# Optimization experiments

Measured on AMD Instinct MI355X. Metric: run time of the kernel, lower is better.

The kernel has to match this reference:

```python
import jax, jax.numpy as jnp
import numpy as np
from jax import lax

B, T, N, D = 4, 12, 1024, 128
C_FRONT = 78           # front/back channel split used by the mixup
X_LAST = T // 2 - 1    # static row index of the last (only effective) mixup call
BS_ST = 6              # block_size of mixup_region_ST
SIGMA = 10.0
LN_EPS = 1e-5


def _mixup_region_ST(graph, y):
    """Faithful jax port of mixup_region_ST(graph_front, x=X_LAST, y, 6, sigma=10).
    graph: [T, N, C_FRONT] float; y: traced int scalar."""
    T_, N_, C_ = graph.shape
    x = X_LAST  # static python int
    y_start = jnp.maximum(y - BS_ST, 0)
    y_end = jnp.minimum(y + 2 * BS_ST, N_)

    # temporal gaussian mix of column y over rows [0, x), written at (x, y)
    xs = jnp.arange(x, dtype=graph.dtype)
    w = jnp.exp(-((xs - (x - 1.0)) ** 2) / (2.0 * SIGMA ** 2))
    w = w / w.sum()
    target = graph[:x, y, :]                      # [x, C]
    mixed_value = (w[:, None] * target).sum(0)    # [C]
    g = lax.dynamic_update_slice(graph, mixed_value[None, None, :], (x, y, 0))

    def mix_write(g_, bs, maxj):
        # average blocks g_[:, j*bs:(j+1)*bs, :] for j in [y_start//bs, y_end//bs)
        j0 = y_start // bs
        j1 = y_end // bs
        jj = jnp.arange(maxj)
        mask = (jj < (j1 - j0)).astype(g_.dtype)              # [maxj]
        cols = jnp.clip((j0 + jj)[:, None] * bs + jnp.arange(bs)[None, :], 0, N_ - 1)
        blocks = g_[:, cols, :]                               # [T, maxj, bs, C]
        mixed = (blocks * mask[None, :, None, None]).sum(1) / (j1 - j0).astype(g_.dtype)
        # torch writes mixed_region.to(torch.uint8) into a float tensor
        mixed = lax.stop_gradient(mixed.astype(jnp.uint8).astype(g_.dtype))
        return lax.dynamic_update_slice(g_, mixed, (0, y, 0))

    # torch resets block_size to 1 when y_end > w - block_size
    return lax.cond(y_end > N_ - BS_ST,
                    lambda g_: mix_write(g_, 1, 3 * BS_ST),
                    lambda g_: mix_write(g_, BS_ST, 4),
                    g)


def _forward(inp, adapt_G, xff_w, xff_b, ff1_w, ff1_b, ff2_w, ff2_b, ln_w, ln_b):
    x_ = inp @ xff_w.T + xff_b                       # [B,T,N,3D]
    q, k, v = jnp.split(x_, 3, axis=-1)
    e = jnp.einsum('btnd,btmd->btnm', q, k) / (D ** 0.5)
    e = e @ adapt_G                                  # [B,T,N,N]
    attn = jax.nn.softmax(e, axis=-1)
    attn_det = lax.stop_gradient(attn)               # self.attention_maps = attn.detach()

    def process(attn_b, val_b):                      # [T,N,N], [T,N,D]
        front = val_b[..., :C_FRONT]
        back = val_b[..., C_FRONT:]
        col_sums = attn_b.sum(axis=1)                # [T, N]
        _, idx = lax.top_k(-col_sums, 2)             # 2 smallest per row, ascending
        # only the last loop iteration's mixup survives in the original code
        y = idx[X_LAST, 1]
        return jnp.concatenate([_mixup_region_ST(front, y), back], axis=-1)

    new_value = jax.vmap(process)(attn_det, v)       # [B,T,N,D]
    vi = attn @ new_value                            # [B,T,N,D]
    h = jax.nn.gelu(vi @ ff1_w.T + ff1_b, approximate=False)
    h = h @ ff2_w.T + ff2_b
    out = h + inp
    mu = out.mean(-1, keepdims=True)
    var = ((out - mu) ** 2).mean(-1, keepdims=True)
    return (out - mu) / jnp.sqrt(var + LN_EPS) * ln_w + ln_b


def setup_inputs() -> dict:
    key = jax.random.key(0)
    ks = jax.random.split(key, 6)
    s = 0.02
    return {
        'input': jax.random.normal(ks[0], (B, T, N, D), jnp.float32),
        'adapt_G': jax.random.normal(ks[1], (N, N), jnp.float32) / np.float32(np.sqrt(N)),
        'xff_w': jax.random.normal(ks[2], (3 * D, D), jnp.float32) * s,
        'xff_b': jnp.zeros((3 * D,), jnp.float32),
        'ff1_w': jax.random.normal(ks[3], (D, D), jnp.float32) * s,
        'ff1_b': jnp.zeros((D,), jnp.float32),
        'ff2_w': jax.random.normal(ks[4], (D, D), jnp.float32) * s,
        'ff2_b': jnp.zeros((D,), jnp.float32),
        'ln_w': jnp.ones((D,), jnp.float32),
        'ln_b': jnp.zeros((D,), jnp.float32),
    }


def reference(input, adapt_G, xff_w, xff_b, ff1_w, ff1_b, ff2_w, ff2_b, ln_w, ln_b):
    return _forward(input, adapt_G, xff_w, xff_b, ff1_w, ff1_b, ff2_w, ff2_b, ln_w, ln_b)
```

## Files before the change

### kernel.cpp

```cpp
#include <hip/hip_runtime.h>
#include <hip/hip_bf16.h>

typedef __attribute__((ext_vector_type(8))) short bf16x8;
typedef __attribute__((ext_vector_type(4))) float f32x4;
typedef unsigned long long ull;

#define MFMA(a,b,c) __builtin_amdgcn_mfma_f32_16x16x32_bf16((a),(b),(c),0,0,0)
#define VMCNT(N) asm volatile("s_waitcnt vmcnt(%0)" :: "i"(N) : "memory")

__device__ __forceinline__ short f2bs(float f){
  union { float f; unsigned u; } x; x.f = f;
  unsigned r = (x.u + 0x7fffu + ((x.u >> 16) & 1u)) >> 16;
  return (short)r;
}
__device__ __forceinline__ float bs2f(short s){
  union { unsigned u; float f; } x; x.u = ((unsigned)(unsigned short)s) << 16;
  return x.f;
}

__device__ __forceinline__ void gl2lds16(const void* g, void* l){
  __builtin_amdgcn_global_load_lds((const __attribute__((address_space(1))) void*)g,
                                   (__attribute__((address_space(3))) void*)l, 16, 0, 0);
}

__device__ __forceinline__ void merge2(ull& a1, ull& a2, ull b1, ull b2){
  ull n1 = min(a1, b1);
  ull n2 = min(max(a1, b1), min(a2, b2));
  a1 = n1; a2 = n2;
}

__global__ __launch_bounds__(256) void prep_kernel(const float* __restrict__ xffw,
                                                   const float* __restrict__ w1,
                                                   const float* __restrict__ w2,
                                                   const float* __restrict__ G,
                                                   short* __restrict__ wqkv_b,
                                                   short* __restrict__ w1_b,
                                                   short* __restrict__ w2_b,
                                                   short* __restrict__ gt){
  __shared__ float tile[32][33];
  int blk = blockIdx.x;
  if (blk >= 1024){
    int i = (blk-1024)*256 + threadIdx.x;
    int stride = 32*256;
    for (int idx = i; idx < 384*128; idx += stride) wqkv_b[idx] = f2bs(xffw[idx]);
    for (int idx = i; idx < 128*128; idx += stride) w1_b[idx] = f2bs(w1[idx]);
    for (int idx = i; idx < 128*128; idx += stride) w2_b[idx] = f2bs(w2[idx]);
    return;
  }
  int bx = blk & 31;
  int by = blk >> 5;
  int tx = threadIdx.x & 31, ty = threadIdx.x >> 5;
  #pragma unroll
  for (int j=0;j<4;j++){
    int n = by*32 + ty + j*8;
    tile[ty+j*8][tx] = G[(size_t)n*1024 + bx*32 + tx];
  }
  __syncthreads();
  #pragma unroll
  for (int j=0;j<4;j++){
    int m = bx*32 + ty + j*8;
    gt[(size_t)m*1024 + by*32 + tx] = f2bs(tile[tx][ty+j*8]);
  }
}

__global__ __launch_bounds__(256,3) void qkv_kernel(const float* __restrict__ inp,
                                                  const short* __restrict__ wqkv,
                                                  const float* __restrict__ bias,
                                                  short* __restrict__ q, short* __restrict__ kT,
                                                  short* __restrict__ nvt){
  __shared__ __align__(16) char smem[49152];
  int w = threadIdx.x >> 6, lane = threadIdx.x & 63;
  int lr = lane & 15, lg = lane >> 4;
  int r0 = blockIdx.x*64;
  int bt = blockIdx.x >> 4;
  int n0 = r0 & 1023;
  int rw = r0 + w*16;
  bf16x8 a[4];
  #pragma unroll
  for (int kc=0;kc<4;kc++){
    const float* ar = inp + (size_t)(rw+lr)*128 + kc*32 + lg*8;
    float4 f0 = *(const float4*)ar;
    float4 f1 = *(const float4*)(ar+4);
    bf16x8 t;
    t[0]=f2bs(f0.x); t[1]=f2bs(f0.y); t[2]=f2bs(f0.z); t[3]=f2bs(f0.w);
    t[4]=f2bs(f1.x); t[5]=f2bs(f1.y); t[6]=f2bs(f1.z); t[7]=f2bs(f1.w);
    a[kc]=t;
  }
  auto stageW = [&](int buf, int kc){
    #pragma unroll
    for (int t=0;t<6;t++){
      int r = (w*6+t)*16 + (lane>>2);
      int s = (lane&3) ^ ((r>>1)&3);
      gl2lds16(wqkv + (size_t)r*128 + kc*32 + s*8,
               smem + buf*24576 + (w*6+t)*1024);
    }
  };
  f32x4 acc[24];
  #pragma unroll
  for (int j=0;j<24;j++) acc[j] = f32x4{0.f,0.f,0.f,0.f};
  stageW(0, 0);
  int cur = 0;
  for (int kc=0; kc<4; kc++){
    if (kc < 3) { stageW(cur^1, kc+1); VMCNT(6); } else { VMCNT(0); }
    __builtin_amdgcn_s_barrier();
    __builtin_amdgcn_sched_barrier(0);
    const char* wb = smem + cur*24576;
    __builtin_amdgcn_s_setprio(1);
    #pragma unroll
    for (int jt=0;jt<24;jt++){
      int j = jt*16 + lr;
      bf16x8 b = *(const bf16x8*)(wb + (size_t)j*64 + ((lg ^ ((lr>>1)&3))*16));
      acc[jt] = MFMA(a[kc], b, acc[jt]);
    }
    __builtin_amdgcn_s_setprio(0);
    __builtin_amdgcn_s_barrier();
    cur ^= 1;
  }
  #pragma unroll
  for (int jt=0;jt<8;jt++){
    float bj = bias[jt*16+lr];
    #pragma unroll
    for (int rr=0;rr<4;rr++)
      q[(size_t)(rw + lg*4 + rr)*128 + jt*16 + lr] = f2bs(acc[jt][rr] + bj);
  }
  __syncthreads();
  short (*tb)[72] = (short(*)[72])smem;
  #pragma unroll
  for (int jt=8;jt<16;jt++){
    int d = (jt-8)*16 + lr;
    float bj = bias[jt*16+lr];
    #pragma unroll
    for (int rr=0;rr<4;rr++) tb[d][w*16 + lg*4 + rr] = f2bs(acc[jt][rr] + bj);
  }
  __syncthreads();
  #pragma unroll
  for (int it=0;it<4;it++){
    int idx = it*256 + threadIdx.x;
    int row = idx >> 3, c8 = (idx & 7)*8;
    *(bf16x8*)(kT + ((size_t)bt*128 + row)*1024 + n0 + c8) = *(const bf16x8*)&tb[row][c8];
  }
  __syncthreads();
  #pragma unroll
  for (int jt=16;jt<24;jt++){
    int c = (jt-16)*16 + lr;
    float bj = bias[jt*16+lr];
    #pragma unroll
    for (int rr=0;rr<4;rr++) tb[c][w*16 + lg*4 + rr] = f2bs(acc[jt][rr] + bj);
  }
  __syncthreads();
  #pragma unroll
  for (int it=0;it<4;it++){
    int idx = it*256 + threadIdx.x;
    int row = idx >> 3, c8 = (idx & 7)*8;
    *(bf16x8*)(nvt + ((size_t)bt*128 + row)*1024 + n0 + c8) = *(const bf16x8*)&tb[row][c8];
  }
}

__global__ __launch_bounds__(256,3) void kg_kernel(const short* __restrict__ gt,
                                                   const short* __restrict__ kT,
                                                   short* __restrict__ kgt){
  __shared__ __align__(16) short gtl[2][64*64];
  __shared__ __align__(16) short ktl[2][128*64];
  int lb = (blockIdx.x & 7)*96 + (blockIdx.x >> 3);
  int bt = lb >> 4;
  int mt = lb & 15;
  int w = threadIdx.x>>6, lane = threadIdx.x&63, lr = lane&15, lg = lane>>4;
  int mblk = mt*64;
  const short* kbase = kT + (size_t)bt*128*1024;
  auto stage = [&](int b, int nc){
    int n0 = nc*64;
    #pragma unroll
    for (int t=0;t<2;t++){
      int row = w*16 + t*8 + (lane>>3);
      int cswz = ((lane&7)*16) ^ ((row&7)<<4);
      gl2lds16(gt + (size_t)(mblk+row)*1024 + n0 + (cswz>>1),
               (char*)gtl[b] + w*2048 + t*1024);
    }
    #pragma unroll
    for (int t=0;t<4;t++){
      int row = w*32 + t*8 + (lane>>3);
      int cswz = ((lane&7)*16) ^ ((row&7)<<4);
      gl2lds16(kbase + (size_t)row*1024 + n0 + (cswz>>1),
               (char*)ktl[b] + w*4096 + t*1024);
    }
  };
  f32x4 acc[8];
  #pragma unroll
  for (int i=0;i<8;i++) acc[i] = f32x4{0.f,0.f,0.f,0.f};
  stage(0, 0);
  int cur = 0;
  for (int nc=0; nc<16; nc++){
    if (nc < 15) { stage(cur^1, nc+1); VMCNT(6); } else { VMCNT(0); }
    __builtin_amdgcn_s_barrier();
    __builtin_amdgcn_sched_barrier(0);
    __builtin_amdgcn_s_setprio(1);
    #pragma unroll
    for (int ks=0;ks<2;ks++){
      int arl = w*16 + lr;
      int acb = ks*64 + lg*16;
      bf16x8 af = *(const bf16x8*)((const char*)gtl[cur] + arl*128 + (acb ^ ((arl&7)<<4)));
      #pragma unroll
      for (int dt=0;dt<8;dt++){
        int brl = dt*16 + lr;
        bf16x8 bf = *(const bf16x8*)((const char*)ktl[cur] + brl*128 + (acb ^ ((brl&7)<<4)));
        acc[dt] = MFMA(af, bf, acc[dt]);
      }
    }
    __builtin_amdgcn_s_setprio(0);
    __builtin_amdgcn_s_barrier();
    cur ^= 1;
  }
  const float SCALE = 0.08838834764831845f;
  int m = mblk + w*16 + lg*4;
  #pragma unroll
  for (int dt=0;dt<8;dt++){
    #pragma unroll
    for (int rr=0;rr<4;rr++){
      kgt[((size_t)(bt*1024 + m + rr))*128 + dt*16 + lr] = f2bs(acc[dt][rr]*SCALE);
    }
  }
}

__global__ __launch_bounds__(256,4) void fused_kernel(const short* __restrict__ q,
                                                      const short* __restrict__ kgt,
                                                      const short* __restrict__ nvt,
                                                      float* __restrict__ zbuf,
                                                      short* __restrict__ pbuf,
                                                      short* __restrict__ vib){
  __shared__ __align__(16) short kgl[64*128];
  __shared__ __align__(16) short nvl[128*64];
  __shared__ __align__(16) short p_lds[4][16][64];
  int lb = (blockIdx.x & 7)*96 + (blockIdx.x >> 3);
  int bt = lb >> 4;
  int rblk = lb & 15;
  int w = threadIdx.x>>6, lane = threadIdx.x&63, lr = lane&15, lg = lane>>4;
  int r0 = rblk*64 + w*16;
  bool is5 = (bt % 12) == 5;
  int bq = bt / 12;
  const short* qrow = q + ((size_t)(bt*1024 + r0 + lr))*128;
  bf16x8 a[4];
  #pragma unroll
  for (int kc=0;kc<4;kc++) a[kc] = *(const bf16x8*)(qrow + kc*32 + lg*8);
  const short* kgb = kgt + (size_t)bt*1024*128;
  const short* nvb = nvt + (size_t)bt*128*1024;
  auto stage_kg = [&](int mc){
    int m0 = mc*64;
    #pragma unroll
    for (int t=0;t<4;t++){
      int row = w*16 + t*4 + (lane>>4);
      int cswz = ((lane&15)*16) ^ ((row&7)<<4);
      gl2lds16(kgb + (size_t)(m0+row)*128 + (cswz>>1),
               (char*)kgl + w*4096 + t*1024);
    }
  };
  auto stage_nv = [&](int mc){
    int m0 = mc*64;
    #pragma unroll
    for (int t=0;t<4;t++){
      int row = w*32 + t*8 + (lane>>3);
      int cswz = ((lane&7)*16) ^ ((row&7)<<4);
      gl2lds16(nvb + (size_t)row*1024 + m0 + (cswz>>1),
               (char*)nvl + w*4096 + t*1024);
    }
  };
  f32x4 acc[8];
  #pragma unroll
  for (int i=0;i<8;i++) acc[i] = f32x4{0.f,0.f,0.f,0.f};
  float zacc[4] = {0.f,0.f,0.f,0.f};
  stage_kg(0);
  stage_nv(0);
  VMCNT(0);
  __builtin_amdgcn_s_barrier();
  __builtin_amdgcn_sched_barrier(0);
  for (int mc=0; mc<16; mc++){
    int m0 = mc*64;
    __builtin_amdgcn_s_setprio(1);
    #pragma unroll
    for (int s=0;s<4;s++){
      f32x4 e = f32x4{0.f,0.f,0.f,0.f};
      #pragma unroll
      for (int kc=0;kc<4;kc++){
        int rl = s*16 + lr;
        int cb = kc*64 + lg*16;
        bf16x8 kb = *(const bf16x8*)((const char*)kgl + rl*256 + (cb ^ ((rl&7)<<4)));
        e = MFMA(a[kc], kb, e);
      }
      #pragma unroll
      for (int rr=0;rr<4;rr++){
        float p = __expf(fminf(e[rr], 60.f));
        zacc[rr] += p;
        p_lds[w][lg*4+rr][s*16+lr] = f2bs(p);
      }
    }
    __builtin_amdgcn_s_setprio(0);
    __builtin_amdgcn_s_barrier();
    if (mc < 15) stage_kg(mc+1);
    if (mc < 15) { VMCNT(4); } else { VMCNT(0); }
    __builtin_amdgcn_s_barrier();
    __builtin_amdgcn_sched_barrier(0);
    bf16x8 pa0 = *(const bf16x8*)&p_lds[w][lr][lg*8];
    bf16x8 pa1 = *(const bf16x8*)&p_lds[w][lr][32+lg*8];
    __builtin_amdgcn_s_setprio(1);
    #pragma unroll
    for (int ct=0; ct<8; ct++){
      int c = ct*16 + lr;
      int mb0 = lg*16;
      int mb1 = 64 + lg*16;
      bf16x8 nb0 = *(const bf16x8*)((const char*)nvl + c*128 + (mb0 ^ ((c&7)<<4)));
      bf16x8 nb1 = *(const bf16x8*)((const char*)nvl + c*128 + (mb1 ^ ((c&7)<<4)));
      acc[ct] = MFMA(pa0, nb0, acc[ct]);
      acc[ct] = MFMA(pa1, nb1, acc[ct]);
    }
    __builtin_amdgcn_s_setprio(0);
    if (is5){
      #pragma unroll
      for (int tt=0; tt<4; tt++){
        int row = tt*4 + (lane>>4);
        int m = (lane&15)*4;
        ull v = *(const ull*)&p_lds[w][row][m];
        *(ull*)(pbuf + ((size_t)bq*1024 + r0 + row)*1024 + m0 + m) = v;
      }
    }
    __builtin_amdgcn_s_barrier();
    if (mc < 15) { stage_nv(mc+1); VMCNT(4); } else { VMCNT(0); }
    __builtin_amdgcn_s_barrier();
    __builtin_amdgcn_sched_barrier(0);
  }
  #pragma unroll
  for (int d=1;d<16;d<<=1){
    #pragma unroll
    for (int rr=0;rr<4;rr++) zacc[rr] += __shfl_xor(zacc[rr], d, 64);
  }
  if (lr==0){
    #pragma unroll
    for (int rr=0;rr<4;rr++) zbuf[(size_t)bt*1024 + r0 + lg*4 + rr] = zacc[rr];
  }
  float inv[4];
  #pragma unroll
  for (int rr=0;rr<4;rr++) inv[rr] = 1.0f/zacc[rr];
  #pragma unroll
  for (int ct=0;ct<8;ct++){
    #pragma unroll
    for (int rr=0;rr<4;rr++){
      vib[((size_t)(bt*1024 + r0 + lg*4 + rr))*128 + ct*16 + lr] = f2bs(acc[ct][rr]*inv[rr]);
    }
  }
}

__global__ __launch_bounds__(256) void colsum_kernel(const short* __restrict__ pbuf,
                                                     const float* __restrict__ zbuf,
                                                     float* __restrict__ csfinal){
  __shared__ float part[4][64];
  int b = blockIdx.x >> 4, mg = blockIdx.x & 15;
  int t = threadIdx.x;
  int mcol = mg*64 + (t & 63);
  int rq = t >> 6;
  const short* pb = pbuf + (size_t)b*1024*1024;
  const float* zb = zbuf + (size_t)(b*12 + 5)*1024;
  float s = 0.f;
  for (int r = rq*256; r < rq*256 + 256; r++){
    s += bs2f(pb[(size_t)r*1024 + mcol]) * (1.0f/zb[r]);
  }
  part[rq][t & 63] = s;
  __syncthreads();
  if (t < 64){
    float cs = (part[0][t] + part[1][t]) + (part[2][t] + part[3][t]);
    csfinal[(size_t)b*1024 + mg*64 + t] = cs;
  }
}

__global__ __launch_bounds__(256) void top2_kernel(const float* __restrict__ csfinal,
                                                   int* __restrict__ yidx){
  __shared__ ull s1[4], s2[4];
  int b = blockIdx.x;
  ull b1 = ~0ull, b2 = ~0ull;
  #pragma unroll
  for (int j=0;j<4;j++){
    int col = j*256 + threadIdx.x;
    float s = csfinal[(size_t)b*1024 + col];
    union { float f; unsigned u; } cv; cv.f = s;
    ull key = ((ull)cv.u << 32) | (unsigned)col;
    merge2(b1, b2, key, ~0ull);
  }
  #pragma unroll
  for (int d=1;d<64;d<<=1){
    ull o1 = __shfl_xor(b1, d, 64);
    ull o2 = __shfl_xor(b2, d, 64);
    merge2(b1, b2, o1, o2);
  }
  int w = threadIdx.x >> 6;
  if ((threadIdx.x & 63) == 0){ s1[w] = b1; s2[w] = b2; }
  __syncthreads();
  if (threadIdx.x == 0){
    ull r1 = s1[0], r2 = s2[0];
    merge2(r1, r2, s1[1], s2[1]);
    merge2(r1, r2, s1[2], s2[2]);
    merge2(r1, r2, s1[3], s2[3]);
    yidx[b] = (int)(r2 & 0xffffffffu);
  }
}

__global__ void nvfixA_kernel(const short* __restrict__ nvt, const int* __restrict__ yidx,
                              float* __restrict__ mixres){
  int bt = blockIdx.x; int b = bt/12, t = bt%12;
  int y = yidx[b];
  int y_start = max(y-6, 0), y_end = min(y+12, 1024);
  int bs, j0, cnt;
  if (y_end > 1024-6){ bs = 1; j0 = y_start; cnt = y_end - y_start; }
  else { bs = 6; j0 = y_start/6; cnt = y_end/6 - j0; }
  int items = bs*78;
  int idx = threadIdx.x;
  if (idx >= items) return;
  int i = idx / 78, c = idx % 78;
  const short* nvb = nvt + (size_t)bt*128*1024;
  float acc = 0.f;
  for (int jj=0;jj<cnt;jj++){
    int col = (j0+jj)*bs + i;
    float gv;
    if (t == 5 && col == y){
      float wsum = 0.f, mv = 0.f;
      #pragma unroll
      for (int tp=0;tp<5;tp++){
        float d = (float)tp - 4.0f;
        float w = __expf(-d*d/200.0f);
        wsum += w;
        mv += w * bs2f(nvt[((size_t)(b*12+tp)*128 + c)*1024 + y]);
      }
      gv = mv / wsum;
    } else {
      gv = bs2f(nvb[(size_t)c*1024 + col]);
    }
    acc += gv;
  }
  mixres[((size_t)bt*6 + i)*78 + c] = acc / (float)cnt;
}

__global__ __launch_bounds__(256) void corr_kernel(const short* __restrict__ q,
                                                   const short* __restrict__ kgt,
                                                   const short* __restrict__ nvt,
                                                   const float* __restrict__ mixres,
                                                   const float* __restrict__ zbuf,
                                                   const int* __restrict__ yidx,
                                                   short* __restrict__ vib){
  __shared__ __align__(16) short kcol[6][128];
  __shared__ float delta[6][78];
  int bt = blockIdx.x >> 2;
  int rc = blockIdx.x & 3;
  int b = bt/12;
  int y = yidx[b];
  int y_end = min(y+12, 1024);
  int bs = (y_end > 1024-6) ? 1 : 6;
  for (int idx = threadIdx.x; idx < 6*128; idx += 256){
    int i = idx >> 7, d = idx & 127;
    kcol[i][d] = (i < bs) ? kgt[((size_t)(bt*1024 + y + i))*128 + d] : (short)0;
  }
  for (int idx = threadIdx.x; idx < 6*78; idx += 256){
    int i = idx / 78, c = idx % 78;
    float dv = 0.f;
    if (i < bs){
      float avg = mixres[((size_t)bt*6 + i)*78 + c];
      int ti = (int)avg;
      unsigned char u = (unsigned char)ti;
      dv = (float)u - bs2f(nvt[((size_t)bt*128 + c)*1024 + (y+i)]);
    }
    delta[i][c] = dv;
  }
  __syncthreads();
  int r = rc*256 + threadIdx.x;
  const short* qr = q + ((size_t)(bt*1024 + r))*128;
  float e[6] = {0.f,0.f,0.f,0.f,0.f,0.f};
  for (int d0 = 0; d0 < 128; d0 += 8){
    bf16x8 qv = *(const bf16x8*)(qr + d0);
    #pragma unroll
    for (int j=0;j<8;j++){
      float qf = bs2f(qv[j]);
      #pragma unroll
      for (int i=0;i<6;i++) e[i] += qf * bs2f(kcol[i][d0+j]);
    }
  }
  float invz = 1.0f / zbuf[(size_t)bt*1024 + r];
  float p[6];
  #pragma unroll
  for (int i=0;i<6;i++) p[i] = (i < bs) ? __expf(fminf(e[i],60.f))*invz : 0.f;
  short* vr = vib + ((size_t)(bt*1024 + r))*128;
  for (int c=0;c<78;c++){
    float dsum = 0.f;
    #pragma unroll
    for (int i=0;i<6;i++) dsum += p[i]*delta[i][c];
    vr[c] = f2bs(bs2f(vr[c]) + dsum);
  }
}

__global__ __launch_bounds__(256,3) void ffn_kernel(const short* __restrict__ vib,
                                                  const float* __restrict__ inp,
                                                  const short* __restrict__ w1b,
                                                  const short* __restrict__ w2b,
                                                  const float* __restrict__ b1,
                                                  const float* __restrict__ b2,
                                                  const float* __restrict__ lnw,
                                                  const float* __restrict__ lnb,
                                                  float* __restrict__ out){
  __shared__ __align__(16) short wl[128*128];
  __shared__ __align__(16) short h_lds[4][16][136];
  int w = threadIdx.x>>6, lane = threadIdx.x&63, lr = lane&15, lg = lane>>4;
  int r0 = blockIdx.x*64 + w*16;
  auto stageW = [&](const short* src){
    #pragma unroll
    for (int t=0;t<8;t++){
      int r = (w*8+t)*4 + (lane>>4);
      int s = (lane&15) ^ (r&7);
      gl2lds16(src + (size_t)r*128 + s*8, (char*)wl + (w*8+t)*1024);
    }
  };
  stageW(w1b);
  bf16x8 a[4];
  #pragma unroll
  for (int kc=0;kc<4;kc++) a[kc] = *(const bf16x8*)(vib + (size_t)(r0+lr)*128 + kc*32 + lg*8);
  __syncthreads();
  f32x4 acc[8];
  #pragma unroll
  for (int i=0;i<8;i++) acc[i] = f32x4{0.f,0.f,0.f,0.f};
  __builtin_amdgcn_s_setprio(1);
  #pragma unroll
  for (int kc=0;kc<4;kc++){
    #pragma unroll
    for (int jt=0;jt<8;jt++){
      bf16x8 b = *(const bf16x8*)((const char*)wl + (size_t)(jt*16+lr)*256 + (((kc*4+lg) ^ (lr&7))*16));
      acc[jt] = MFMA(a[kc], b, acc[jt]);
    }
  }
  __builtin_amdgcn_s_setprio(0);
  #pragma unroll
  for (int jt=0;jt<8;jt++){
    float bj = b1[jt*16+lr];
    #pragma unroll
    for (int rr=0;rr<4;rr++){
      float x = acc[jt][rr] + bj;
      float g = 0.5f*x*(1.0f + erff(x*0.70710678118654752f));
      h_lds[w][lg*4+rr][jt*16+lr] = f2bs(g);
    }
  }
  __syncthreads();
  stageW(w2b);
  bf16x8 ha[4];
  #pragma unroll
  for (int kc=0;kc<4;kc++) ha[kc] = *(const bf16x8*)&h_lds[w][lr][kc*32 + lg*8];
  __syncthreads();
  f32x4 acc2[8];
  #pragma unroll
  for (int i=0;i<8;i++) acc2[i] = f32x4{0.f,0.f,0.f,0.f};
  __builtin_amdgcn_s_setprio(1);
  #pragma unroll
  for (int kc=0;kc<4;kc++){
    #pragma unroll
    for (int jt=0;jt<8;jt++){
      bf16x8 b = *(const bf16x8*)((const char*)wl + (size_t)(jt*16+lr)*256 + (((kc*4+lg) ^ (lr&7))*16));
      acc2[jt] = MFMA(ha[kc], b, acc2[jt]);
    }
  }
  __builtin_amdgcn_s_setprio(0);
  float xv[8][4];
  #pragma unroll
  for (int jt=0;jt<8;jt++){
    float bj = b2[jt*16+lr];
    #pragma unroll
    for (int rr=0;rr<4;rr++){
      xv[jt][rr] = acc2[jt][rr] + bj + inp[(size_t)(r0 + lg*4 + rr)*128 + jt*16 + lr];
    }
  }
  float mu[4], rstd[4];
  #pragma unroll
  for (int rr=0;rr<4;rr++){
    float s = 0.f;
    #pragma unroll
    for (int jt=0;jt<8;jt++) s += xv[jt][rr];
    #pragma unroll
    for (int m=1;m<16;m<<=1) s += __shfl_xor(s, m, 64);
    mu[rr] = s * (1.0f/128.0f);
  }
  #pragma unroll
  for (int rr=0;rr<4;rr++){
    float s = 0.f;
    #pragma unroll
    for (int jt=0;jt<8;jt++){ float d = xv[jt][rr]-mu[rr]; s += d*d; }
    #pragma unroll
    for (int m=1;m<16;m<<=1) s += __shfl_xor(s, m, 64);
    rstd[rr] = rsqrtf(s * (1.0f/128.0f) + 1e-5f);
  }
  #pragma unroll
  for (int jt=0;jt<8;jt++){
    int col = jt*16 + lr;
    float lw = lnw[col], lb = lnb[col];
    #pragma unroll
    for (int rr=0;rr<4;rr++){
      out[(size_t)(r0 + lg*4 + rr)*128 + col] = (xv[jt][rr]-mu[rr])*rstd[rr]*lw + lb;
    }
  }
}

extern "C" void kernel_launch(void* const* d_in, const int* in_sizes, int n_in,
                              void* d_out, int out_size, void* d_ws, size_t ws_size,
                              hipStream_t stream) {
  (void)in_sizes; (void)n_in; (void)out_size;
  const float* inp  = (const float*)d_in[0];
  const float* G    = (const float*)d_in[1];
  const float* xffw = (const float*)d_in[2];
  const float* xffb = (const float*)d_in[3];
  const float* w1   = (const float*)d_in[4];
  const float* b1   = (const float*)d_in[5];
  const float* w2   = (const float*)d_in[6];
  const float* b2   = (const float*)d_in[7];
  const float* lnw  = (const float*)d_in[8];
  const float* lnb  = (const float*)d_in[9];
  float* out = (float*)d_out;
  char* ws = (char*)d_ws;

  size_t off = 0;
  auto take = [&](size_t bytes)->char*{ char* p = ws + off; off += (bytes + 255) & ~(size_t)255; return p; };
  short* wqkv_b = (short*)take(384*128*2);
  short* gt_b   = (short*)take((size_t)1024*1024*2);
  short* w1_b   = (short*)take(128*128*2);
  short* w2_b   = (short*)take(128*128*2);
  short* qb     = (short*)take((size_t)48*1024*128*2);
  short* kTb    = (short*)take((size_t)48*128*1024*2);
  short* nvt    = (short*)take((size_t)48*128*1024*2);
  short* kgt    = (short*)take((size_t)48*1024*128*2);
  float* zbuf   = (float*)take((size_t)48*1024*4);
  short* pbuf   = (short*)take((size_t)4*1024*1024*2);
  float* csfin  = (float*)take((size_t)4*1024*4);
  int*   yidx   = (int*)take(256);
  float* mixres = (float*)take((size_t)48*6*78*4);
  short* vibuf  = (short*)take((size_t)48*1024*128*2);
  if (off > ws_size) return;

  prep_kernel<<<dim3(1056), dim3(256), 0, stream>>>(xffw, w1, w2, G, wqkv_b, w1_b, w2_b, gt_b);
  qkv_kernel<<<dim3(768), dim3(256), 0, stream>>>(inp, wqkv_b, xffb, qb, kTb, nvt);
  kg_kernel<<<dim3(768), dim3(256), 0, stream>>>(gt_b, kTb, kgt);
  fused_kernel<<<dim3(768), dim3(256), 0, stream>>>(qb, kgt, nvt, zbuf, pbuf, vibuf);
  colsum_kernel<<<dim3(64), dim3(256), 0, stream>>>(pbuf, zbuf, csfin);
  top2_kernel<<<dim3(4), dim3(256), 0, stream>>>(csfin, yidx);
  nvfixA_kernel<<<dim3(48), dim3(512), 0, stream>>>(nvt, yidx, mixres);
  corr_kernel<<<dim3(192), dim3(256), 0, stream>>>(qb, kgt, nvt, mixres, zbuf, yidx, vibuf);
  ffn_kernel<<<dim3(768), dim3(256), 0, stream>>>(vibuf, inp, w1_b, w2_b, b1, b2, lnw, lnb, out);
}
```

Baseline: 153.5 us.

## Halve waves per block in fused attention kernel, each wave handling two row groups

The fused attention kernel now runs 128 threads (2 waves) per block instead of 4. Each wave computes 32 rows as two 16-row MFMA groups, so every K/V fragment read from LDS is reused twice. This cuts LDS reads per MFMA and barrier participants per block, and each wave issues twice as many staging loads. The P scratch buffer is now XOR-swizzled to avoid bank conflicts. In exchange, register pressure roughly doubles (two accumulator sets) and occupancy per CU drops, with launch bounds lowered to 2.

```diff
diff --git a/kernel.cpp b/kernel.cpp
--- a/kernel.cpp
+++ b/kernel.cpp
@@ -221,7 +221,7 @@
   }
 }
 
-__global__ __launch_bounds__(256,4) void fused_kernel(const short* __restrict__ q,
+__global__ __launch_bounds__(128,2) void fused_kernel(const short* __restrict__ q,
                                                       const short* __restrict__ kgt,
                                                       const short* __restrict__ nvt,
                                                       float* __restrict__ zbuf,
@@ -229,44 +229,51 @@
                                                       short* __restrict__ vib){
   __shared__ __align__(16) short kgl[64*128];
   __shared__ __align__(16) short nvl[128*64];
-  __shared__ __align__(16) short p_lds[4][16][64];
+  __shared__ __align__(16) char  p_raw[8192];
   int lb = (blockIdx.x & 7)*96 + (blockIdx.x >> 3);
   int bt = lb >> 4;
   int rblk = lb & 15;
   int w = threadIdx.x>>6, lane = threadIdx.x&63, lr = lane&15, lg = lane>>4;
-  int r0 = rblk*64 + w*16;
+  int r0 = rblk*64 + w*32;
   bool is5 = (bt % 12) == 5;
   int bq = bt / 12;
-  const short* qrow = q + ((size_t)(bt*1024 + r0 + lr))*128;
-  bf16x8 a[4];
-  #pragma unroll
-  for (int kc=0;kc<4;kc++) a[kc] = *(const bf16x8*)(qrow + kc*32 + lg*8);
+  bf16x8 a[2][4];
+  #pragma unroll
+  for (int g=0;g<2;g++){
+    const short* qrow = q + ((size_t)(bt*1024 + r0 + g*16 + lr))*128;
+    #pragma unroll
+    for (int kc=0;kc<4;kc++) a[g][kc] = *(const bf16x8*)(qrow + kc*32 + lg*8);
+  }
   const short* kgb = kgt + (size_t)bt*1024*128;
   const short* nvb = nvt + (size_t)bt*128*1024;
   auto stage_kg = [&](int mc){
     int m0 = mc*64;
     #pragma unroll
-    for (int t=0;t<4;t++){
-      int row = w*16 + t*4 + (lane>>4);
+    for (int t=0;t<8;t++){
+      int row = w*32 + t*4 + (lane>>4);
       int cswz = ((lane&15)*16) ^ ((row&7)<<4);
       gl2lds16(kgb + (size_t)(m0+row)*128 + (cswz>>1),
-               (char*)kgl + w*4096 + t*1024);
+               (char*)kgl + w*8192 + t*1024);
     }
   };
   auto stage_nv = [&](int mc){
     int m0 = mc*64;
     #pragma unroll
-    for (int t=0;t<4;t++){
-      int row = w*32 + t*8 + (lane>>3);
+    for (int t=0;t<8;t++){
+      int row = w*64 + t*8 + (lane>>3);
       int cswz = ((lane&7)*16) ^ ((row&7)<<4);
       gl2lds16(nvb + (size_t)row*1024 + m0 + (cswz>>1),
-               (char*)nvl + w*4096 + t*1024);
+               (char*)nvl + w*8192 + t*1024);
     }
   };
-  f32x4 acc[8];
-  #pragma unroll
-  for (int i=0;i<8;i++) acc[i] = f32x4{0.f,0.f,0.f,0.f};
-  float zacc[4] = {0.f,0.f,0.f,0.f};
+  f32x4 acc[2][8];
+  #pragma unroll
+  for (int g=0;g<2;g++)
+    #pragma unroll
+    for (int i=0;i<8;i++) acc[g][i] = f32x4{0.f,0.f,0.f,0.f};
+  float zacc[2][4] = {{0.f,0.f,0.f,0.f},{0.f,0.f,0.f,0.f}};
+  char* pw0 = p_raw + (w*2+0)*2048;
+  char* pw1 = p_raw + (w*2+1)*2048;
   stage_kg(0);
   stage_nv(0);
   VMCNT(0);
@@ -277,29 +284,41 @@
     __builtin_amdgcn_s_setprio(1);
     #pragma unroll
     for (int s=0;s<4;s++){
-      f32x4 e = f32x4{0.f,0.f,0.f,0.f};
+      f32x4 e0 = f32x4{0.f,0.f,0.f,0.f};
+      f32x4 e1 = f32x4{0.f,0.f,0.f,0.f};
       #pragma unroll
       for (int kc=0;kc<4;kc++){
         int rl = s*16 + lr;
         int cb = kc*64 + lg*16;
         bf16x8 kb = *(const bf16x8*)((const char*)kgl + rl*256 + (cb ^ ((rl&7)<<4)));
-        e = MFMA(a[kc], kb, e);
+        e0 = MFMA(a[0][kc], kb, e0);
+        e1 = MFMA(a[1][kc], kb, e1);
       }
       #pragma unroll
       for (int rr=0;rr<4;rr++){
-        float p = __expf(fminf(e[rr], 60.f));
-        zacc[rr] += p;
-        p_lds[w][lg*4+rr][s*16+lr] = f2bs(p);
+        int row = lg*4+rr;
+        int boff = ((row*128 + (s*16+lr)*2) ^ ((row&7)<<4));
+        float p0 = __expf(fminf(e0[rr], 60.f));
+        float p1 = __expf(fminf(e1[rr], 60.f));
+        zacc[0][rr] += p0;
+        zacc[1][rr] += p1;
+        *(short*)(pw0 + boff) = f2bs(p0);
+        *(short*)(pw1 + boff) = f2bs(p1);
       }
     }
     __builtin_amdgcn_s_setprio(0);
     __builtin_amdgcn_s_barrier();
     if (mc < 15) stage_kg(mc+1);
-    if (mc < 15) { VMCNT(4); } else { VMCNT(0); }
+    if (mc < 15) { VMCNT(8); } else { VMCNT(0); }
     __builtin_amdgcn_s_barrier();
     __builtin_amdgcn_sched_barrier(0);
-    bf16x8 pa0 = *(const bf16x8*)&p_lds[w][lr][lg*8];
-    bf16x8 pa1 = *(const bf16x8*)&p_lds[w][lr][32+lg*8];
+    bf16x8 pa[2][2];
+    #pragma unroll
+    for (int g=0;g<2;g++){
+      char* pw = g ? pw1 : pw0;
+      pa[g][0] = *(const bf16x8*)(pw + ((lr*128 + lg*16) ^ ((lr&7)<<4)));
+      pa[g][1] = *(const bf16x8*)(pw + ((lr*128 + 64 + lg*16) ^ ((lr&7)<<4)));
+    }
     __builtin_amdgcn_s_setprio(1);
     #pragma unroll
     for (int ct=0; ct<8; ct++){
@@ -308,41 +327,55 @@
       int mb1 = 64 + lg*16;
       bf16x8 nb0 = *(const bf16x8*)((const char*)nvl + c*128 + (mb0 ^ ((c&7)<<4)));
       bf16x8 nb1 = *(const bf16x8*)((const char*)nvl + c*128 + (mb1 ^ ((c&7)<<4)));
-      acc[ct] = MFMA(pa0, nb0, acc[ct]);
-      acc[ct] = MFMA(pa1, nb1, acc[ct]);
+      acc[0][ct] = MFMA(pa[0][0], nb0, acc[0][ct]);
+      acc[0][ct] = MFMA(pa[0][1], nb1, acc[0][ct]);
+      acc[1][ct] = MFMA(pa[1][0], nb0, acc[1][ct]);
+      acc[1][ct] = MFMA(pa[1][1], nb1, acc[1][ct]);
     }
     __builtin_amdgcn_s_setprio(0);
     if (is5){
       #pragma unroll
-      for (int tt=0; tt<4; tt++){
-        int row = tt*4 + (lane>>4);
-        int m = (lane&15)*4;
-        ull v = *(const ull*)&p_lds[w][row][m];
-        *(ull*)(pbuf + ((size_t)bq*1024 + r0 + row)*1024 + m0 + m) = v;
+      for (int g=0;g<2;g++){
+        char* pw = g ? pw1 : pw0;
+        #pragma unroll
+        for (int tt=0; tt<4; tt++){
+          int row = tt*4 + (lane>>4);
+          int m = (lane&15)*4;
+          ull v = *(const ull*)(pw + ((row*128 + m*2) ^ ((row&7)<<4)));
+          *(ull*)(pbuf + ((size_t)bq*1024 + r0 + g*16 + row)*1024 + m0 + m) = v;
+        }
       }
     }
     __builtin_amdgcn_s_barrier();
-    if (mc < 15) { stage_nv(mc+1); VMCNT(4); } else { VMCNT(0); }
+    if (mc < 15) { stage_nv(mc+1); VMCNT(8); } else { VMCNT(0); }
     __builtin_amdgcn_s_barrier();
     __builtin_amdgcn_sched_barrier(0);
   }
   #pragma unroll
-  for (int d=1;d<16;d<<=1){
-    #pragma unroll
-    for (int rr=0;rr<4;rr++) zacc[rr] += __shfl_xor(zacc[rr], d, 64);
+  for (int g=0;g<2;g++){
+    #pragma unroll
+    for (int d=1;d<16;d<<=1){
+      #pragma unroll
+      for (int rr=0;rr<4;rr++) zacc[g][rr] += __shfl_xor(zacc[g][rr], d, 64);
+    }
   }
   if (lr==0){
     #pragma unroll
-    for (int rr=0;rr<4;rr++) zbuf[(size_t)bt*1024 + r0 + lg*4 + rr] = zacc[rr];
-  }
-  float inv[4];
-  #pragma unroll
-  for (int rr=0;rr<4;rr++) inv[rr] = 1.0f/zacc[rr];
-  #pragma unroll
-  for (int ct=0;ct<8;ct++){
-    #pragma unroll
-    for (int rr=0;rr<4;rr++){
-      vib[((size_t)(bt*1024 + r0 + lg*4 + rr))*128 + ct*16 + lr] = f2bs(acc[ct][rr]*inv[rr]);
+    for (int g=0;g<2;g++)
+      #pragma unroll
+      for (int rr=0;rr<4;rr++) zbuf[(size_t)bt*1024 + r0 + g*16 + lg*4 + rr] = zacc[g][rr];
+  }
+  #pragma unroll
+  for (int g=0;g<2;g++){
+    float inv[4];
+    #pragma unroll
+    for (int rr=0;rr<4;rr++) inv[rr] = 1.0f/zacc[g][rr];
+    #pragma unroll
+    for (int ct=0;ct<8;ct++){
+      #pragma unroll
+      for (int rr=0;rr<4;rr++){
+        vib[((size_t)(bt*1024 + r0 + g*16 + lg*4 + rr))*128 + ct*16 + lr] = f2bs(acc[g][ct][rr]*inv[rr]);
+      }
     }
   }
 }
@@ -636,7 +669,7 @@
   prep_kernel<<<dim3(1056), dim3(256), 0, stream>>>(xffw, w1, w2, G, wqkv_b, w1_b, w2_b, gt_b);
   qkv_kernel<<<dim3(768), dim3(256), 0, stream>>>(inp, wqkv_b, xffb, qb, kTb, nvt);
   kg_kernel<<<dim3(768), dim3(256), 0, stream>>>(gt_b, kTb, kgt);
-  fused_kernel<<<dim3(768), dim3(256), 0, stream>>>(qb, kgt, nvt, zbuf, pbuf, vibuf);
+  fused_kernel<<<dim3(768), dim3(128), 0, stream>>>(qb, kgt, nvt, zbuf, pbuf, vibuf);
   colsum_kernel<<<dim3(64), dim3(256), 0, stream>>>(pbuf, zbuf, csfin);
   top2_kernel<<<dim3(4), dim3(256), 0, stream>>>(csfin, yidx);
   nvfixA_kernel<<<dim3(48), dim3(512), 0, stream>>>(nvt, yidx, mixres);
```

After: 153.5 us. No clear change (-0.0%).
